# Optimization experiments

Hardware: AMD Instinct MI355X
Metric: run time of the kernel (lower is better)

The kernel has to match this reference:

```python
import jax, jax.numpy as jnp
import numpy as np

N_NODES = 384
HEIGHT = 60
C = 128
N_LAYERS = 4
EDGE_CH = 5
EPS = 1e-5


def _create_board(base=0):
    board = np.zeros((8, 8), dtype=int)
    num = 0
    for i in range(0, 8, 2):
        for j in range(0, 8, 2):
            board[i, j] = num
            board[i, j + 1] = num + 1
            board[i + 1, j] = num + 2
            board[i + 1, j + 1] = num + 3
            num += 4
    return np.fliplr(np.rot90(board, k=2)) + base * 64


def _get_neighbors(face, i, j):
    nb = []
    if i > 0: nb.append(face[i - 1, j])
    if i < 7: nb.append(face[i + 1, j])
    if j > 0: nb.append(face[i, j - 1])
    if j < 7: nb.append(face[i, j + 1])
    return nb


def _get_boundary_neighbors(faces):
    boundary = {i: [] for i in range(N_NODES)}
    connections = [(0,'left',3,'right','same'),(0,'up',5,'down','same'),(0,'right',1,'left','same'),(0,'down',4,'up','same'),(1,'left',0,'right','same'),(1,'up',5,'right','reverse'),(1,'right',2,'left','same'),(1,'down',4,'right','same'),(2,'left',1,'right','same'),(2,'up',5,'up','reverse'),(2,'right',3,'left','same'),(2,'down',4,'down','reverse'),(3,'left',2,'right','same'),(3,'up',5,'left','same'),(3,'right',0,'left','same'),(3,'down',4,'left','reverse'),(4,'left',3,'down','reverse'),(4,'up',0,'down','same'),(4,'right',1,'down','same'),(4,'down',2,'down','reverse'),(5,'left',3,'up','same'),(5,'up',2,'up','reverse'),(5,'right',1,'up','reverse'),(5,'down',0,'up','same')]

    def coord(index, edge, reverse):
        if edge == 'left':  c = (index, 0)
        elif edge == 'right': c = (index, 7)
        elif edge == 'up':  c = (0, index)
        else:               c = (7, index)
        if reverse:
            c = (7 - index, c[1]) if edge in ('left', 'right') else (c[0], 7 - index)
        return c

    for f1, e1, f2, e2, order in connections:
        for i in range(8):
            c1 = coord(i, e1, False)
            c2 = coord(i, e2, order == 'reverse')
            boundary[faces[f1][c1]].append(faces[f2][c2])
            boundary[faces[f2][c2]].append(faces[f1][c1])
    return boundary


def _create_edge_index():
    adj = np.zeros((N_NODES, N_NODES), dtype=int)
    faces = [_create_board(base=i) for i in range(6)]
    for face in faces:
        for i in range(8):
            for j in range(8):
                idx = face[i, j]
                for nb in _get_neighbors(face, i, j):
                    adj[idx, nb] = 1
                    adj[nb, idx] = 1
    for idx, nbs in _get_boundary_neighbors(faces).items():
        for nb in nbs:
            adj[idx, nb] = 1
            adj[nb, idx] = 1
    for i in range(N_NODES):
        for j in range(i + 1, N_NODES):
            if i // 4 == j // 4:
                adj[i, j] = 1
                adj[j, i] = 1
    np.fill_diagonal(adj, 1)  # self_loop
    return np.array(np.nonzero(adj))  # (2, E), E = 3072


def setup_inputs() -> dict:
    key = jax.random.key(0)
    k_x, k_ew, k_cw = jax.random.split(key, 3)
    ei = _create_edge_index()
    # edge_attr = sin/cos of lat/lon diffs + is_same_spectral (5 features)
    rng = np.random.default_rng(0)
    lat = np.radians(rng.uniform(-90.0, 90.0, N_NODES))
    lon = np.radians(rng.uniform(0.0, 360.0, N_NODES))
    lat_d = lat[ei[0]] - lat[ei[1]]
    lon_d = lon[ei[0]] - lon[ei[1]]
    same = (ei[0] // 4 == ei[1] // 4).astype(np.float32)
    ea = np.stack([np.sin(lat_d), np.cos(lat_d), np.sin(lon_d), np.cos(lon_d), same], axis=1).astype(np.float32)
    x = jax.random.normal(k_x, (N_NODES, C, HEIGHT), dtype=jnp.float32)
    return {
        "x": x,
        "edge_attr": jnp.asarray(ea),
        "edge_w": jax.random.normal(k_ew, (N_LAYERS, C, EDGE_CH), dtype=jnp.float32) * 0.3,
        "edge_b": jnp.zeros((N_LAYERS, C), dtype=jnp.float32),
        "conv_w": jax.random.normal(k_cw, (N_LAYERS, C, 3 * C), dtype=jnp.float32) / np.float32(np.sqrt(3 * C)),
        "ln_g": jnp.ones((N_LAYERS, C, HEIGHT), dtype=jnp.float32),
        "ln_b": jnp.zeros((N_LAYERS, C, HEIGHT), dtype=jnp.float32),
        "edge_index": jnp.asarray(ei, dtype=jnp.int32),
    }


def _layer(x, edge_index, edge_attr, ew, eb, cw, g, b):
    # x: (N, C, H); edge_index: (2, E)
    src, dst = edge_index[0], edge_index[1]
    h_i = x[dst]                                 # (E, C, H) target (x_i)
    h_j = x[src]                                 # (E, C, H) source (x_j)
    e = edge_attr @ ew.T + eb                    # (E, C) edge_linear
    e = jnp.broadcast_to(e[:, :, None], h_i.shape)
    h = jnp.concatenate([h_i, h_j - h_i, e], axis=1)   # (E, 3C, H)
    h = jnp.einsum('ekh,ck->ech', h, cw)                # kernel-size-1 Conv1d
    mu = jnp.mean(h, axis=(1, 2), keepdims=True)        # LayerNorm over (C, H)
    var = jnp.mean((h - mu) ** 2, axis=(1, 2), keepdims=True)
    h = (h - mu) * jax.lax.rsqrt(var + EPS) * g + b
    h = jax.nn.relu(h)
    return jax.ops.segment_sum(h, dst, num_segments=N_NODES)  # aggr='add'


def reference(x, edge_attr, edge_w, edge_b, conv_w, ln_g, ln_b, edge_index):
    for l in range(N_LAYERS):
        x = _layer(x, edge_index, edge_attr, edge_w[l], edge_b[l], conv_w[l], ln_g[l], ln_b[l])
    return x  # (384, C, 60)
```

## Files before the change

kernel.cpp:

```cpp
#include <hip/hip_runtime.h>
#include <hip/hip_bf16.h>

#define NN 384
#define CC 128
#define HH 60
#define NEL (CC*HH)
#define NLAYERS 4

typedef _Float16 f16x4 __attribute__((ext_vector_type(4)));
typedef float f32x4 __attribute__((ext_vector_type(4)));

__device__ __forceinline__ void cvt2(float v, _Float16& hi, _Float16& lo) {
    hi = (_Float16)v; lo = (_Float16)(v - (float)hi);
}
__device__ __forceinline__ int nmap(int bid) { return ((bid & 7) * 48) + (bid >> 3); }

__global__ __launch_bounds__(256) void k_setup(
    const float* __restrict__ cw, const float* __restrict__ ew, const float* __restrict__ eb,
    const float* __restrict__ lg, const float* __restrict__ lb, const int* __restrict__ ei, int E,
    float* __restrict__ M3, float* __restrict__ v3,
    _Float16* __restrict__ wfh, _Float16* __restrict__ wfl,
    float* __restrict__ gp, float* __restrict__ bp,
    int* __restrict__ off, int* __restrict__ ssrc, int* __restrict__ seid)
{
    int bid = blockIdx.x, t = threadIdx.x;
    if (bid == 0) {
        __shared__ int cnt[NN + 1];
        __shared__ int cur[NN];
        for (int i = t; i < NN + 1; i += 256) cnt[i] = 0;
        __syncthreads();
        const int* dstp = ei + E;
        for (int e = t; e < E; e += 256) atomicAdd(&cnt[dstp[e] + 1], 1);
        __syncthreads();
        if (t == 0) { int s = 0; for (int i = 0; i <= NN; i++) { s += cnt[i]; cnt[i] = s; } }
        __syncthreads();
        for (int i = t; i < NN + 1; i += 256) off[i] = cnt[i];
        for (int i = t; i < NN; i += 256) cur[i] = cnt[i];
        __syncthreads();
        for (int e = t; e < E; e += 256) {
            int d = dstp[e];
            int p = atomicAdd(&cur[d], 1);
            ssrc[p] = ei[e];
            seid[p] = e;
        }
    } else if (bid < 5) {
        if (t < CC) {
            int l = bid - 1, c = t;
            const float* wrow = cw + (l * CC + c) * (3 * CC) + 2 * CC;
            const float* ewl = ew + l * CC * 5;
            const float* ebl = eb + l * CC;
            float m0 = 0, m1 = 0, m2 = 0, m3 = 0, m4 = 0, v = 0;
            for (int k = 0; k < CC; k++) {
                float wv = wrow[k];
                const float* e5 = ewl + k * 5;
                m0 = fmaf(wv, e5[0], m0); m1 = fmaf(wv, e5[1], m1); m2 = fmaf(wv, e5[2], m2);
                m3 = fmaf(wv, e5[3], m3); m4 = fmaf(wv, e5[4], m4);
                v  = fmaf(wv, ebl[k], v);
            }
            float* mo = M3 + (l * CC + c) * 5;
            mo[0] = m0; mo[1] = m1; mo[2] = m2; mo[3] = m3; mo[4] = m4;
            v3[l * CC + c] = v;
        }
    } else if (bid < 21) {
        int wid = ((bid - 5) << 2) + (t >> 6);
        int lane = t & 63;
        int l = wid >> 4;
        const float* cwl = cw + l * CC * 3 * CC;
        int r = ((wid & 15) << 4) + (lane & 15);
#pragma unroll
        for (int kt = 0; kt < 8; kt++) {
#pragma unroll
            for (int j = 0; j < 4; j++) {
                int k = (kt << 4) + ((lane >> 4) << 2) + j;
                float wv;
                if (r < 128) wv = cwl[r * 384 + k] - cwl[r * 384 + 128 + k];
                else         wv = cwl[(r - 128) * 384 + 128 + k];
                _Float16 hi, lo; cvt2(wv, hi, lo);
                int idx = (wid * 8 + kt) * 256 + lane * 4 + j;
                wfh[idx] = hi; wfl[idx] = lo;
            }
        }
    } else if (bid < 141) {
        int gidx = ((bid - 21) << 8) + t;
        int l = gidx / NEL, q = gidx - l * NEL;
        int c = q & 127, h = q >> 7;
        gp[gidx] = lg[l * NEL + c * HH + h];
        bp[gidx] = lb[l * NEL + c * HH + h];
    }
}

__device__ __forceinline__ void mm_core8(char* XhB, char* XlB,
                                         const _Float16* __restrict__ wfhL,
                                         const _Float16* __restrict__ wflL,
                                         float* __restrict__ Aout, float* __restrict__ Bout,
                                         int n, int w, int lane)
{
    f16x4 whv[2][8];
#pragma unroll
    for (int nt = 0; nt < 2; nt++)
#pragma unroll
        for (int kt = 0; kt < 8; kt++)
            whv[nt][kt] = *(const f16x4*)(wfhL + (((((w << 1) + nt) << 3) + kt) << 8) + (lane << 2));

    f32x4 acc[4][2];
#pragma unroll
    for (int mt = 0; mt < 4; mt++)
#pragma unroll
        for (int nt = 0; nt < 2; nt++) acc[mt][nt] = (f32x4){0.f, 0.f, 0.f, 0.f};

#pragma unroll
    for (int ks = 0; ks < 8; ks++) {
        f16x4 wlv[2];
#pragma unroll
        for (int nt = 0; nt < 2; nt++)
            wlv[nt] = *(const f16x4*)(wflL + (((((w << 1) + nt) << 3) + ks) << 8) + (lane << 2));
        f16x4 ah[4], al[4];
#pragma unroll
        for (int mt = 0; mt < 4; mt++) {
            int h = (mt << 4) + (lane & 15);
            int o = (h << 8) + (((ks << 5) + ((lane >> 4) << 3)) ^ ((h & 7) << 4));
            ah[mt] = *(const f16x4*)(XhB + o);
            al[mt] = *(const f16x4*)(XlB + o);
        }
#pragma unroll
        for (int mt = 0; mt < 4; mt++)
#pragma unroll
            for (int nt = 0; nt < 2; nt++) {
                acc[mt][nt] = __builtin_amdgcn_mfma_f32_16x16x16f16(ah[mt], whv[nt][ks], acc[mt][nt], 0, 0, 0);
                acc[mt][nt] = __builtin_amdgcn_mfma_f32_16x16x16f16(al[mt], whv[nt][ks], acc[mt][nt], 0, 0, 0);
                acc[mt][nt] = __builtin_amdgcn_mfma_f32_16x16x16f16(ah[mt], wlv[nt], acc[mt][nt], 0, 0, 0);
            }
    }
    float* Out = ((w < 4) ? Aout : Bout) + n * NEL + ((w & 3) << 5);
#pragma unroll
    for (int mt = 0; mt < 4; mt++) {
        int hb = (mt << 4) + ((lane >> 4) << 2);
#pragma unroll
        for (int nt = 0; nt < 2; nt++) {
            int rl = (nt << 4) + (lane & 15);
#pragma unroll
            for (int reg = 0; reg < 4; reg++) {
                int h = hb + reg;
                if (h < HH) Out[h * 128 + rl] = acc[mt][nt][reg];
            }
        }
    }
}

__global__ __launch_bounds__(512, 4) void k_mm0(const float* __restrict__ x,
                                                const _Float16* __restrict__ wfhL,
                                                const _Float16* __restrict__ wflL,
                                                float* __restrict__ Aout, float* __restrict__ Bout)
{
    __shared__ __align__(16) char smem[32768];
    char* XhB = smem;
    char* XlB = smem + 16384;
    int n = nmap(blockIdx.x), t = threadIdx.x;
    int w = t >> 6, lane = t & 63;

    const float* xn = x + n * NEL;
    for (int p = t; p < 3840; p += 512) {
        int q = p << 1;
        int c = q & 127, h = q >> 7;
        float v0 = xn[c * HH + h], v1 = xn[(c + 1) * HH + h];
        _Float16 h0, l0, h1, l1; cvt2(v0, h0, l0); cvt2(v1, h1, l1);
        int o = (h << 8) + ((c << 1) ^ ((h & 7) << 4));
        union { _Float16 f[2]; unsigned u; } ph, pl;
        ph.f[0] = h0; ph.f[1] = h1; pl.f[0] = l0; pl.f[1] = l1;
        *(unsigned*)(XhB + o) = ph.u;
        *(unsigned*)(XlB + o) = pl.u;
    }
    if (t < 64) {
        int h = 60 + (t >> 4), ch = t & 15;
        int o = (h << 8) + ((ch << 4) ^ ((h & 7) << 4));
        *(uint4*)(XhB + o) = make_uint4(0, 0, 0, 0);
        *(uint4*)(XlB + o) = make_uint4(0, 0, 0, 0);
    }
    __syncthreads();
    mm_core8(XhB, XlB, wfhL, wflL, Aout, Bout, n, w, lane);
}

template<bool LAST>
__global__ __launch_bounds__(512, 4) void k_fused(
    const float* __restrict__ Ain, const float* __restrict__ Bin,
    const float* __restrict__ ea,
    const float* __restrict__ M3l, const float* __restrict__ v3l,
    const float* __restrict__ gpl, const float* __restrict__ bpl,
    const int* __restrict__ off, const int* __restrict__ ssrc, const int* __restrict__ seid,
    const _Float16* __restrict__ wfhL, const _Float16* __restrict__ wflL,
    float* __restrict__ Aout, float* __restrict__ Bout)
{
    __shared__ __align__(16) char smem[32768];
    int d = nmap(blockIdx.x), t = threadIdx.x;
    int w = t >> 6, lane = t & 63;
    float* c3all = (float*)smem;
    float* red   = c3all + 1024;

    int j0 = off[d], j1 = off[d + 1], cnt = j1 - j0;

    for (int idx = t; idx < (cnt << 7); idx += 512) {
        int j = idx >> 7, c = idx & 127;
        int eid = seid[j0 + j];
        const float* eap = ea + eid * 5;
        const float* m = M3l + c * 5;
        c3all[idx] = v3l[c] + m[0]*eap[0] + m[1]*eap[1] + m[2]*eap[2] + m[3]*eap[3] + m[4]*eap[4];
    }

    float areg[15], greg[15], breg[15], accv[15];
    const float* Ad = Ain + d * NEL;
#pragma unroll
    for (int i = 0; i < 15; i++) {
        int p = t + (i << 9);
        areg[i] = Ad[p]; greg[i] = gpl[p]; breg[i] = bpl[p];
        accv[i] = 0.f;
    }
    const int cch = t & 127;
    __syncthreads();

    for (int j = 0; j < cnt; j++) {
        const float* Bs = Bin + ssrc[j0 + j] * NEL;
        float cc = c3all[(j << 7) + cch];
        float bv[15];
        float sum = 0.f, sq = 0.f;
#pragma unroll
        for (int i = 0; i < 15; i++) {
            float v = areg[i] + Bs[t + (i << 9)] + cc;
            bv[i] = v;
            sum += v;
            sq = fmaf(v, v, sq);
        }
#pragma unroll
        for (int o = 32; o; o >>= 1) { sum += __shfl_xor(sum, o); sq += __shfl_xor(sq, o); }
        int jb = j & 1;
        if (lane == 0) { red[jb * 16 + w * 2] = sum; red[jb * 16 + w * 2 + 1] = sq; }
        __syncthreads();
        float fs = 0.f, fq = 0.f;
#pragma unroll
        for (int k = 0; k < 8; k++) { fs += red[jb * 16 + k * 2]; fq += red[jb * 16 + k * 2 + 1]; }
        float mu = fs * (1.0f / NEL);
        float var = fq * (1.0f / NEL) - mu * mu;
        float rs = rsqrtf(var + 1e-5f);
#pragma unroll
        for (int i = 0; i < 15; i++) {
            float nx = (bv[i] - mu) * rs * greg[i] + breg[i];
            accv[i] += fmaxf(nx, 0.f);
        }
    }

    if (LAST) {
        __syncthreads();
        float* xt = (float*)smem;
        int hb0 = t >> 7;
#pragma unroll
        for (int i = 0; i < 15; i++)
            xt[cch * 61 + hb0 + (i << 2)] = accv[i];
        __syncthreads();
        for (int o2 = t; o2 < NEL; o2 += 512) {
            int c2 = o2 / 60, h2 = o2 - c2 * 60;
            Aout[d * NEL + o2] = xt[c2 * 61 + h2];
        }
    } else {
        __syncthreads();
        char* XhB = smem;
        char* XlB = smem + 16384;
        int hb0 = t >> 7;
#pragma unroll
        for (int i = 0; i < 15; i++) {
            int h = hb0 + (i << 2);
            int o = (h << 8) + ((cch << 1) ^ ((h & 7) << 4));
            _Float16 hi, lo; cvt2(accv[i], hi, lo);
            *(_Float16*)(XhB + o) = hi;
            *(_Float16*)(XlB + o) = lo;
        }
        if (t < 64) {
            int h = 60 + (t >> 4), ch = t & 15;
            int o = (h << 8) + ((ch << 4) ^ ((h & 7) << 4));
            *(uint4*)(XhB + o) = make_uint4(0, 0, 0, 0);
            *(uint4*)(XlB + o) = make_uint4(0, 0, 0, 0);
        }
        __syncthreads();
        mm_core8(XhB, XlB, wfhL, wflL, Aout, Bout, d, w, lane);
    }
}

extern "C" void kernel_launch(void* const* d_in, const int* in_sizes, int n_in,
                              void* d_out, int out_size, void* d_ws, size_t ws_size,
                              hipStream_t stream) {
    const float* x  = (const float*)d_in[0];
    const float* ea = (const float*)d_in[1];
    const float* ew = (const float*)d_in[2];
    const float* eb = (const float*)d_in[3];
    const float* cw = (const float*)d_in[4];
    const float* lg = (const float*)d_in[5];
    const float* lb = (const float*)d_in[6];
    const int*   ei = (const int*)d_in[7];
    int E = in_sizes[7] / 2;
    float* out = (float*)d_out;

    float* wsf = (float*)d_ws;
    float* A0 = wsf;
    float* B0 = A0 + NN * NEL;
    float* A1 = B0 + NN * NEL;
    float* B1 = A1 + NN * NEL;
    float* gp = B1 + NN * NEL;
    float* bp = gp + NLAYERS * NEL;
    float* M3 = bp + NLAYERS * NEL;
    float* v3 = M3 + NLAYERS * 640;
    _Float16* wfh = (_Float16*)(v3 + NLAYERS * 128);
    _Float16* wfl = wfh + NLAYERS * 32768;
    int* off  = (int*)(wfl + NLAYERS * 32768);
    int* ssrc = off + (NN + 1);
    int* seid = ssrc + E;

    k_setup<<<141, 256, 0, stream>>>(cw, ew, eb, lg, lb, ei, E,
                                     M3, v3, wfh, wfl, gp, bp, off, ssrc, seid);
    k_mm0<<<NN, 512, 0, stream>>>(x, wfh, wfl, A0, B0);

    k_fused<false><<<NN, 512, 0, stream>>>(A0, B0, ea, M3 + 0 * 640, v3 + 0 * 128,
                                           gp + 0 * NEL, bp + 0 * NEL, off, ssrc, seid,
                                           wfh + 1 * 32768, wfl + 1 * 32768, A1, B1);
    k_fused<false><<<NN, 512, 0, stream>>>(A1, B1, ea, M3 + 1 * 640, v3 + 1 * 128,
                                           gp + 1 * NEL, bp + 1 * NEL, off, ssrc, seid,
                                           wfh + 2 * 32768, wfl + 2 * 32768, A0, B0);
    k_fused<false><<<NN, 512, 0, stream>>>(A0, B0, ea, M3 + 2 * 640, v3 + 2 * 128,
                                           gp + 2 * NEL, bp + 2 * NEL, off, ssrc, seid,
                                           wfh + 3 * 32768, wfl + 3 * 32768, A1, B1);
    k_fused<true><<<NN, 512, 0, stream>>>(A1, B1, ea, M3 + 3 * 640, v3 + 3 * 128,
                                          gp + 3 * NEL, bp + 3 * NEL, off, ssrc, seid,
                                          wfh, wfl, out, out);
}
```

Baseline: 199.8 us.

## Merge all layer kernels into one persistent kernel with grid barriers

Replaces the setup, initial matmul and four per-layer fused kernels with a single persistent kernel of 384 blocks. The blocks synchronise through atomic-counter grid barriers in global memory, with the counters reset by a memset. The aim is to remove kernel launch gaps and tail effects between the six dependent launches. In exchange, all 384 blocks must be co-resident for the spin barriers not to deadlock, and each barrier adds atomic spin-wait latency.

```diff
diff --git a/kernel.cpp b/kernel.cpp
--- a/kernel.cpp
+++ b/kernel.cpp
@@ -15,29 +15,108 @@
 }
 __device__ __forceinline__ int nmap(int bid) { return ((bid & 7) * 48) + (bid >> 3); }
 
-__global__ __launch_bounds__(256) void k_setup(
-    const float* __restrict__ cw, const float* __restrict__ ew, const float* __restrict__ eb,
-    const float* __restrict__ lg, const float* __restrict__ lb, const int* __restrict__ ei, int E,
+__device__ __forceinline__ void gbar(int* bar, int idx) {
+    __syncthreads();
+    if (threadIdx.x == 0) {
+        __threadfence();
+        atomicAdd(&bar[idx], 1);
+        while (__hip_atomic_load(&bar[idx], __ATOMIC_RELAXED, __HIP_MEMORY_SCOPE_AGENT) < NN)
+            __builtin_amdgcn_s_sleep(2);
+        __threadfence();
+    }
+    __syncthreads();
+}
+
+__device__ __forceinline__ void mm_core8(char* XhB, char* XlB,
+                                         const _Float16* __restrict__ wfhL,
+                                         const _Float16* __restrict__ wflL,
+                                         float* __restrict__ Aout, float* __restrict__ Bout,
+                                         int n, int w, int lane)
+{
+    f16x4 whv[2][8];
+#pragma unroll
+    for (int nt = 0; nt < 2; nt++)
+#pragma unroll
+        for (int kt = 0; kt < 8; kt++)
+            whv[nt][kt] = *(const f16x4*)(wfhL + (((((w << 1) + nt) << 3) + kt) << 8) + (lane << 2));
+
+    f32x4 acc[4][2];
+#pragma unroll
+    for (int mt = 0; mt < 4; mt++)
+#pragma unroll
+        for (int nt = 0; nt < 2; nt++) acc[mt][nt] = (f32x4){0.f, 0.f, 0.f, 0.f};
+
+#pragma unroll
+    for (int ks = 0; ks < 8; ks++) {
+        f16x4 wlv[2];
+#pragma unroll
+        for (int nt = 0; nt < 2; nt++)
+            wlv[nt] = *(const f16x4*)(wflL + (((((w << 1) + nt) << 3) + ks) << 8) + (lane << 2));
+        f16x4 ah[4], al[4];
+#pragma unroll
+        for (int mt = 0; mt < 4; mt++) {
+            int h = (mt << 4) + (lane & 15);
+            int o = (h << 8) + (((ks << 5) + ((lane >> 4) << 3)) ^ ((h & 7) << 4));
+            ah[mt] = *(const f16x4*)(XhB + o);
+            al[mt] = *(const f16x4*)(XlB + o);
+        }
+#pragma unroll
+        for (int mt = 0; mt < 4; mt++)
+#pragma unroll
+            for (int nt = 0; nt < 2; nt++) {
+                acc[mt][nt] = __builtin_amdgcn_mfma_f32_16x16x16f16(ah[mt], whv[nt][ks], acc[mt][nt], 0, 0, 0);
+                acc[mt][nt] = __builtin_amdgcn_mfma_f32_16x16x16f16(al[mt], whv[nt][ks], acc[mt][nt], 0, 0, 0);
+                acc[mt][nt] = __builtin_amdgcn_mfma_f32_16x16x16f16(ah[mt], wlv[nt], acc[mt][nt], 0, 0, 0);
+            }
+    }
+    float* Out = ((w < 4) ? Aout : Bout) + n * NEL + ((w & 3) << 5);
+#pragma unroll
+    for (int mt = 0; mt < 4; mt++) {
+        int hb = (mt << 4) + ((lane >> 4) << 2);
+#pragma unroll
+        for (int nt = 0; nt < 2; nt++) {
+            int rl = (nt << 4) + (lane & 15);
+#pragma unroll
+            for (int reg = 0; reg < 4; reg++) {
+                int h = hb + reg;
+                if (h < HH) Out[h * 128 + rl] = acc[mt][nt][reg];
+            }
+        }
+    }
+}
+
+__global__ __launch_bounds__(512, 4) void mega(
+    const float* __restrict__ x, const float* __restrict__ ea,
+    const float* __restrict__ ew, const float* __restrict__ eb,
+    const float* __restrict__ cw, const float* __restrict__ lg,
+    const float* __restrict__ lb, const int* __restrict__ ei, int E,
+    float* __restrict__ out,
+    float* __restrict__ A0, float* __restrict__ B0,
+    float* __restrict__ A1, float* __restrict__ B1,
+    float* __restrict__ gp, float* __restrict__ bp,
     float* __restrict__ M3, float* __restrict__ v3,
     _Float16* __restrict__ wfh, _Float16* __restrict__ wfl,
-    float* __restrict__ gp, float* __restrict__ bp,
-    int* __restrict__ off, int* __restrict__ ssrc, int* __restrict__ seid)
+    int* __restrict__ off, int* __restrict__ ssrc, int* __restrict__ seid,
+    int* __restrict__ bar)
 {
-    int bid = blockIdx.x, t = threadIdx.x;
+    __shared__ __align__(16) char smem[33024];
+    const int bid = blockIdx.x, t = threadIdx.x;
+    const int w = t >> 6, lane = t & 63;
+
     if (bid == 0) {
-        __shared__ int cnt[NN + 1];
-        __shared__ int cur[NN];
-        for (int i = t; i < NN + 1; i += 256) cnt[i] = 0;
+        int* cnt = (int*)smem;
+        int* cur = cnt + NN + 1;
+        for (int i = t; i < NN + 1; i += 512) cnt[i] = 0;
         __syncthreads();
         const int* dstp = ei + E;
-        for (int e = t; e < E; e += 256) atomicAdd(&cnt[dstp[e] + 1], 1);
+        for (int e = t; e < E; e += 512) atomicAdd(&cnt[dstp[e] + 1], 1);
         __syncthreads();
         if (t == 0) { int s = 0; for (int i = 0; i <= NN; i++) { s += cnt[i]; cnt[i] = s; } }
         __syncthreads();
-        for (int i = t; i < NN + 1; i += 256) off[i] = cnt[i];
-        for (int i = t; i < NN; i += 256) cur[i] = cnt[i];
-        __syncthreads();
-        for (int e = t; e < E; e += 256) {
+        for (int i = t; i < NN + 1; i += 512) off[i] = cnt[i];
+        for (int i = t; i < NN; i += 512) cur[i] = cnt[i];
+        __syncthreads();
+        for (int e = t; e < E; e += 512) {
             int d = dstp[e];
             int p = atomicAdd(&cur[d], 1);
             ssrc[p] = ei[e];
@@ -61,9 +140,8 @@
             mo[0] = m0; mo[1] = m1; mo[2] = m2; mo[3] = m3; mo[4] = m4;
             v3[l * CC + c] = v;
         }
-    } else if (bid < 21) {
-        int wid = ((bid - 5) << 2) + (t >> 6);
-        int lane = t & 63;
+    } else if (bid < 13) {
+        int wid = ((bid - 5) << 3) + w;
         int l = wid >> 4;
         const float* cwl = cw + l * CC * 3 * CC;
         int r = ((wid & 15) << 4) + (lane & 15);
@@ -80,197 +158,30 @@
                 wfh[idx] = hi; wfl[idx] = lo;
             }
         }
-    } else if (bid < 141) {
-        int gidx = ((bid - 21) << 8) + t;
+    } else if (bid < 73) {
+        int gidx = ((bid - 13) << 9) + t;
         int l = gidx / NEL, q = gidx - l * NEL;
         int c = q & 127, h = q >> 7;
         gp[gidx] = lg[l * NEL + c * HH + h];
         bp[gidx] = lb[l * NEL + c * HH + h];
     }
-}
-
-__device__ __forceinline__ void mm_core8(char* XhB, char* XlB,
-                                         const _Float16* __restrict__ wfhL,
-                                         const _Float16* __restrict__ wflL,
-                                         float* __restrict__ Aout, float* __restrict__ Bout,
-                                         int n, int w, int lane)
-{
-    f16x4 whv[2][8];
-#pragma unroll
-    for (int nt = 0; nt < 2; nt++)
-#pragma unroll
-        for (int kt = 0; kt < 8; kt++)
-            whv[nt][kt] = *(const f16x4*)(wfhL + (((((w << 1) + nt) << 3) + kt) << 8) + (lane << 2));
-
-    f32x4 acc[4][2];
-#pragma unroll
-    for (int mt = 0; mt < 4; mt++)
-#pragma unroll
-        for (int nt = 0; nt < 2; nt++) acc[mt][nt] = (f32x4){0.f, 0.f, 0.f, 0.f};
-
-#pragma unroll
-    for (int ks = 0; ks < 8; ks++) {
-        f16x4 wlv[2];
-#pragma unroll
-        for (int nt = 0; nt < 2; nt++)
-            wlv[nt] = *(const f16x4*)(wflL + (((((w << 1) + nt) << 3) + ks) << 8) + (lane << 2));
-        f16x4 ah[4], al[4];
-#pragma unroll
-        for (int mt = 0; mt < 4; mt++) {
-            int h = (mt << 4) + (lane & 15);
-            int o = (h << 8) + (((ks << 5) + ((lane >> 4) << 3)) ^ ((h & 7) << 4));
-            ah[mt] = *(const f16x4*)(XhB + o);
-            al[mt] = *(const f16x4*)(XlB + o);
-        }
-#pragma unroll
-        for (int mt = 0; mt < 4; mt++)
-#pragma unroll
-            for (int nt = 0; nt < 2; nt++) {
-                acc[mt][nt] = __builtin_amdgcn_mfma_f32_16x16x16f16(ah[mt], whv[nt][ks], acc[mt][nt], 0, 0, 0);
-                acc[mt][nt] = __builtin_amdgcn_mfma_f32_16x16x16f16(al[mt], whv[nt][ks], acc[mt][nt], 0, 0, 0);
-                acc[mt][nt] = __builtin_amdgcn_mfma_f32_16x16x16f16(ah[mt], wlv[nt], acc[mt][nt], 0, 0, 0);
-            }
-    }
-    float* Out = ((w < 4) ? Aout : Bout) + n * NEL + ((w & 3) << 5);
-#pragma unroll
-    for (int mt = 0; mt < 4; mt++) {
-        int hb = (mt << 4) + ((lane >> 4) << 2);
-#pragma unroll
-        for (int nt = 0; nt < 2; nt++) {
-            int rl = (nt << 4) + (lane & 15);
-#pragma unroll
-            for (int reg = 0; reg < 4; reg++) {
-                int h = hb + reg;
-                if (h < HH) Out[h * 128 + rl] = acc[mt][nt][reg];
-            }
-        }
-    }
-}
-
-__global__ __launch_bounds__(512, 4) void k_mm0(const float* __restrict__ x,
-                                                const _Float16* __restrict__ wfhL,
-                                                const _Float16* __restrict__ wflL,
-                                                float* __restrict__ Aout, float* __restrict__ Bout)
-{
-    __shared__ __align__(16) char smem[32768];
-    char* XhB = smem;
-    char* XlB = smem + 16384;
-    int n = nmap(blockIdx.x), t = threadIdx.x;
-    int w = t >> 6, lane = t & 63;
-
-    const float* xn = x + n * NEL;
-    for (int p = t; p < 3840; p += 512) {
-        int q = p << 1;
-        int c = q & 127, h = q >> 7;
-        float v0 = xn[c * HH + h], v1 = xn[(c + 1) * HH + h];
-        _Float16 h0, l0, h1, l1; cvt2(v0, h0, l0); cvt2(v1, h1, l1);
-        int o = (h << 8) + ((c << 1) ^ ((h & 7) << 4));
-        union { _Float16 f[2]; unsigned u; } ph, pl;
-        ph.f[0] = h0; ph.f[1] = h1; pl.f[0] = l0; pl.f[1] = l1;
-        *(unsigned*)(XhB + o) = ph.u;
-        *(unsigned*)(XlB + o) = pl.u;
-    }
-    if (t < 64) {
-        int h = 60 + (t >> 4), ch = t & 15;
-        int o = (h << 8) + ((ch << 4) ^ ((h & 7) << 4));
-        *(uint4*)(XhB + o) = make_uint4(0, 0, 0, 0);
-        *(uint4*)(XlB + o) = make_uint4(0, 0, 0, 0);
-    }
-    __syncthreads();
-    mm_core8(XhB, XlB, wfhL, wflL, Aout, Bout, n, w, lane);
-}
-
-template<bool LAST>
-__global__ __launch_bounds__(512, 4) void k_fused(
-    const float* __restrict__ Ain, const float* __restrict__ Bin,
-    const float* __restrict__ ea,
-    const float* __restrict__ M3l, const float* __restrict__ v3l,
-    const float* __restrict__ gpl, const float* __restrict__ bpl,
-    const int* __restrict__ off, const int* __restrict__ ssrc, const int* __restrict__ seid,
-    const _Float16* __restrict__ wfhL, const _Float16* __restrict__ wflL,
-    float* __restrict__ Aout, float* __restrict__ Bout)
-{
-    __shared__ __align__(16) char smem[32768];
-    int d = nmap(blockIdx.x), t = threadIdx.x;
-    int w = t >> 6, lane = t & 63;
-    float* c3all = (float*)smem;
-    float* red   = c3all + 1024;
-
-    int j0 = off[d], j1 = off[d + 1], cnt = j1 - j0;
-
-    for (int idx = t; idx < (cnt << 7); idx += 512) {
-        int j = idx >> 7, c = idx & 127;
-        int eid = seid[j0 + j];
-        const float* eap = ea + eid * 5;
-        const float* m = M3l + c * 5;
-        c3all[idx] = v3l[c] + m[0]*eap[0] + m[1]*eap[1] + m[2]*eap[2] + m[3]*eap[3] + m[4]*eap[4];
-    }
-
-    float areg[15], greg[15], breg[15], accv[15];
-    const float* Ad = Ain + d * NEL;
-#pragma unroll
-    for (int i = 0; i < 15; i++) {
-        int p = t + (i << 9);
-        areg[i] = Ad[p]; greg[i] = gpl[p]; breg[i] = bpl[p];
-        accv[i] = 0.f;
-    }
-    const int cch = t & 127;
-    __syncthreads();
-
-    for (int j = 0; j < cnt; j++) {
-        const float* Bs = Bin + ssrc[j0 + j] * NEL;
-        float cc = c3all[(j << 7) + cch];
-        float bv[15];
-        float sum = 0.f, sq = 0.f;
-#pragma unroll
-        for (int i = 0; i < 15; i++) {
-            float v = areg[i] + Bs[t + (i << 9)] + cc;
-            bv[i] = v;
-            sum += v;
-            sq = fmaf(v, v, sq);
-        }
-#pragma unroll
-        for (int o = 32; o; o >>= 1) { sum += __shfl_xor(sum, o); sq += __shfl_xor(sq, o); }
-        int jb = j & 1;
-        if (lane == 0) { red[jb * 16 + w * 2] = sum; red[jb * 16 + w * 2 + 1] = sq; }
-        __syncthreads();
-        float fs = 0.f, fq = 0.f;
-#pragma unroll
-        for (int k = 0; k < 8; k++) { fs += red[jb * 16 + k * 2]; fq += red[jb * 16 + k * 2 + 1]; }
-        float mu = fs * (1.0f / NEL);
-        float var = fq * (1.0f / NEL) - mu * mu;
-        float rs = rsqrtf(var + 1e-5f);
-#pragma unroll
-        for (int i = 0; i < 15; i++) {
-            float nx = (bv[i] - mu) * rs * greg[i] + breg[i];
-            accv[i] += fmaxf(nx, 0.f);
-        }
-    }
-
-    if (LAST) {
-        __syncthreads();
-        float* xt = (float*)smem;
-        int hb0 = t >> 7;
-#pragma unroll
-        for (int i = 0; i < 15; i++)
-            xt[cch * 61 + hb0 + (i << 2)] = accv[i];
-        __syncthreads();
-        for (int o2 = t; o2 < NEL; o2 += 512) {
-            int c2 = o2 / 60, h2 = o2 - c2 * 60;
-            Aout[d * NEL + o2] = xt[c2 * 61 + h2];
-        }
-    } else {
-        __syncthreads();
+    gbar(bar, 0);
+
+    {
         char* XhB = smem;
         char* XlB = smem + 16384;
-        int hb0 = t >> 7;
-#pragma unroll
-        for (int i = 0; i < 15; i++) {
-            int h = hb0 + (i << 2);
-            int o = (h << 8) + ((cch << 1) ^ ((h & 7) << 4));
-            _Float16 hi, lo; cvt2(accv[i], hi, lo);
-            *(_Float16*)(XhB + o) = hi;
-            *(_Float16*)(XlB + o) = lo;
+        int n = nmap(bid);
+        const float* xn = x + n * NEL;
+        for (int p = t; p < 3840; p += 512) {
+            int q = p << 1;
+            int c = q & 127, h = q >> 7;
+            float v0 = xn[c * HH + h], v1 = xn[(c + 1) * HH + h];
+            _Float16 h0, l0, h1, l1; cvt2(v0, h0, l0); cvt2(v1, h1, l1);
+            int o = (h << 8) + ((c << 1) ^ ((h & 7) << 4));
+            union { _Float16 f[2]; unsigned u; } ph, pl;
+            ph.f[0] = h0; ph.f[1] = h1; pl.f[0] = l0; pl.f[1] = l1;
+            *(unsigned*)(XhB + o) = ph.u;
+            *(unsigned*)(XlB + o) = pl.u;
         }
         if (t < 64) {
             int h = 60 + (t >> 4), ch = t & 15;
@@ -279,7 +190,111 @@
             *(uint4*)(XlB + o) = make_uint4(0, 0, 0, 0);
         }
         __syncthreads();
-        mm_core8(XhB, XlB, wfhL, wflL, Aout, Bout, d, w, lane);
+        mm_core8(XhB, XlB, wfh, wfl, A0, B0, n, w, lane);
+    }
+    gbar(bar, 1);
+
+    const int d = nmap(bid);
+    const int j0 = off[d], j1 = off[d + 1], cnt = j1 - j0;
+    const int cch = t & 127;
+
+    for (int l = 0; l < NLAYERS; l++) {
+        const float* Ain = (l & 1) ? A1 : A0;
+        const float* Bin = (l & 1) ? B1 : B0;
+        float* Aout      = (l & 1) ? A0 : A1;
+        float* Bout      = (l & 1) ? B0 : B1;
+        const float* M3l = M3 + l * 640;
+        const float* v3l = v3 + l * 128;
+        const float* gpl = gp + l * NEL;
+        const float* bpl = bp + l * NEL;
+
+        float* c3all = (float*)smem;
+        float* red   = c3all + 1024;
+
+        for (int idx = t; idx < (cnt << 7); idx += 512) {
+            int j = idx >> 7, c = idx & 127;
+            int eid = seid[j0 + j];
+            const float* eap = ea + eid * 5;
+            const float* m = M3l + c * 5;
+            c3all[idx] = v3l[c] + m[0]*eap[0] + m[1]*eap[1] + m[2]*eap[2] + m[3]*eap[3] + m[4]*eap[4];
+        }
+
+        float areg[15], greg[15], breg[15], accv[15];
+        const float* Ad = Ain + d * NEL;
+#pragma unroll
+        for (int i = 0; i < 15; i++) {
+            int p = t + (i << 9);
+            areg[i] = Ad[p]; greg[i] = gpl[p]; breg[i] = bpl[p];
+            accv[i] = 0.f;
+        }
+        __syncthreads();
+
+        for (int j = 0; j < cnt; j++) {
+            const float* Bs = Bin + ssrc[j0 + j] * NEL;
+            float cc = c3all[(j << 7) + cch];
+            float bv[15];
+            float sum = 0.f, sq = 0.f;
+#pragma unroll
+            for (int i = 0; i < 15; i++) {
+                float v = areg[i] + Bs[t + (i << 9)] + cc;
+                bv[i] = v;
+                sum += v;
+                sq = fmaf(v, v, sq);
+            }
+#pragma unroll
+            for (int o = 32; o; o >>= 1) { sum += __shfl_xor(sum, o); sq += __shfl_xor(sq, o); }
+            int jb = j & 1;
+            if (lane == 0) { red[jb * 16 + w * 2] = sum; red[jb * 16 + w * 2 + 1] = sq; }
+            __syncthreads();
+            float fs = 0.f, fq = 0.f;
+#pragma unroll
+            for (int k = 0; k < 8; k++) { fs += red[jb * 16 + k * 2]; fq += red[jb * 16 + k * 2 + 1]; }
+            float mu = fs * (1.0f / NEL);
+            float var = fq * (1.0f / NEL) - mu * mu;
+            float rs = rsqrtf(var + 1e-5f);
+#pragma unroll
+            for (int i = 0; i < 15; i++) {
+                float nx = (bv[i] - mu) * rs * greg[i] + breg[i];
+                accv[i] += fmaxf(nx, 0.f);
+            }
+        }
+
+        if (l == NLAYERS - 1) {
+            __syncthreads();
+            float* xt = (float*)smem;
+            int hb0 = t >> 7;
+#pragma unroll
+            for (int i = 0; i < 15; i++)
+                xt[cch * 61 + hb0 + (i << 2)] = accv[i];
+            __syncthreads();
+            for (int o2 = t; o2 < NEL; o2 += 512) {
+                int c2 = o2 / 60, h2 = o2 - c2 * 60;
+                out[d * NEL + o2] = xt[c2 * 61 + h2];
+            }
+        } else {
+            __syncthreads();
+            char* XhB = smem;
+            char* XlB = smem + 16384;
+            int hb0 = t >> 7;
+#pragma unroll
+            for (int i = 0; i < 15; i++) {
+                int h = hb0 + (i << 2);
+                int o = (h << 8) + ((cch << 1) ^ ((h & 7) << 4));
+                _Float16 hi, lo; cvt2(accv[i], hi, lo);
+                *(_Float16*)(XhB + o) = hi;
+                *(_Float16*)(XlB + o) = lo;
+            }
+            if (t < 64) {
+                int h = 60 + (t >> 4), ch = t & 15;
+                int o = (h << 8) + ((ch << 4) ^ ((h & 7) << 4));
+                *(uint4*)(XhB + o) = make_uint4(0, 0, 0, 0);
+                *(uint4*)(XlB + o) = make_uint4(0, 0, 0, 0);
+            }
+            __syncthreads();
+            mm_core8(XhB, XlB, wfh + (l + 1) * 32768, wfl + (l + 1) * 32768,
+                     Aout, Bout, d, w, lane);
+            gbar(bar, 2 + l);
+        }
     }
 }
 
@@ -311,21 +326,11 @@
     int* off  = (int*)(wfl + NLAYERS * 32768);
     int* ssrc = off + (NN + 1);
     int* seid = ssrc + E;
-
-    k_setup<<<141, 256, 0, stream>>>(cw, ew, eb, lg, lb, ei, E,
-                                     M3, v3, wfh, wfl, gp, bp, off, ssrc, seid);
-    k_mm0<<<NN, 512, 0, stream>>>(x, wfh, wfl, A0, B0);
-
-    k_fused<false><<<NN, 512, 0, stream>>>(A0, B0, ea, M3 + 0 * 640, v3 + 0 * 128,
-                                           gp + 0 * NEL, bp + 0 * NEL, off, ssrc, seid,
-                                           wfh + 1 * 32768, wfl + 1 * 32768, A1, B1);
-    k_fused<false><<<NN, 512, 0, stream>>>(A1, B1, ea, M3 + 1 * 640, v3 + 1 * 128,
-                                           gp + 1 * NEL, bp + 1 * NEL, off, ssrc, seid,
-                                           wfh + 2 * 32768, wfl + 2 * 32768, A0, B0);
-    k_fused<false><<<NN, 512, 0, stream>>>(A0, B0, ea, M3 + 2 * 640, v3 + 2 * 128,
-                                           gp + 2 * NEL, bp + 2 * NEL, off, ssrc, seid,
-                                           wfh + 3 * 32768, wfl + 3 * 32768, A1, B1);
-    k_fused<true><<<NN, 512, 0, stream>>>(A1, B1, ea, M3 + 3 * 640, v3 + 3 * 128,
-                                          gp + 3 * NEL, bp + 3 * NEL, off, ssrc, seid,
-                                          wfh, wfl, out, out);
-}
+    int* bar  = seid + E;
+
+    hipMemsetAsync(bar, 0, 8 * sizeof(int), stream);
+
+    mega<<<NN, 512, 0, stream>>>(x, ea, ew, eb, cw, lg, lb, ei, E, out,
+                                 A0, B0, A1, B1, gp, bp, M3, v3, wfh, wfl,
+                                 off, ssrc, seid, bar);
+}
```

After: 485.2 us. 2.43x slower.
